# Optimization experiments

Hardware: AMD Instinct MI355X
Metric: run time of the kernel (lower is better)

The kernel has to match this reference:

```python
import jax, jax.numpy as jnp
import numpy as np

N_NODES = 50000
N_EDGES = 800000
D_IN = 128
D_OUT = 128


def setup_inputs() -> dict:
    key = jax.random.key(0)
    k1, k2, k3, k4, k5, k6 = jax.random.split(key, 6)
    embeddings = jax.random.normal(k1, (N_NODES, D_IN), dtype=jnp.float32)
    # kaiming-normal-style scale for the weight
    weight = jax.random.normal(k2, (D_IN, D_OUT), dtype=jnp.float32) * np.sqrt(2.0 / D_IN)
    bias = jax.random.normal(k3, (D_OUT,), dtype=jnp.float32) * 0.01
    edge_val = jax.random.uniform(k4, (N_EDGES,), dtype=jnp.float32)
    edge_row = jax.random.randint(k5, (N_EDGES,), 0, N_NODES, dtype=jnp.int32)
    edge_col = jax.random.randint(k6, (N_EDGES,), 0, N_NODES, dtype=jnp.int32)
    return {
        "embeddings": embeddings,
        "weight": weight,
        "bias": bias,
        "edge_val": edge_val,
        "edge_row": edge_row,
        "edge_col": edge_col,
    }


def reference(embeddings, weight, bias, edge_val, edge_row, edge_col):
    # support = X @ W  -> [N, D_OUT]
    support = jnp.matmul(embeddings, weight)
    # spmm(adj, support): for each edge (r, c, v): out[r] += v * support[c]
    msgs = edge_val[:, None] * support[edge_col]          # [E, D_OUT]
    out = jax.ops.segment_sum(msgs, edge_row, num_segments=embeddings.shape[0])
    return out + bias
```

## Files before the change

kernel.cpp:

```cpp
#include <hip/hip_runtime.h>

#define N_NODES 50000
#define N_EDGES 800000
#define D 128
#define NB 782
#define CHUNK 4096

#define S_OFF      0u
#define GCNT_OFF   12800000u
#define START_OFF  12803200u
#define GCUR_OFF   12806400u
#define OFFS_OFF   12809600u
#define RECS_OFF   13009664u
#define CSR_OFF    19409664u
#define WS_NEEDED  (CSR_OFF + (size_t)N_EDGES * 4u)

__device__ __forceinline__ unsigned bf16_rne(float f) {
    unsigned u = __float_as_uint(f);
    return (u + 0x7fffu + ((u >> 16) & 1u)) >> 16;
}

__global__ __launch_bounds__(512) void gc_gemm(const float* __restrict__ X,
                                               const float* __restrict__ W,
                                               unsigned* __restrict__ Sb) {
    __shared__ float4 LW[4096];
    const int t = threadIdx.x;
    const float4* W4 = (const float4*)W;
    #pragma unroll
    for (int i = 0; i < 8; ++i) LW[t + i * 512] = W4[t + i * 512];
    __syncthreads();

    const int rg = t >> 5;
    const int cg = t & 31;
    const int row0 = blockIdx.x * 64 + rg * 4;
    if (row0 >= N_NODES) return;

    const float4* x0 = (const float4*)(X + (size_t)(row0 + 0) * D);
    const float4* x1 = (const float4*)(X + (size_t)(row0 + 1) * D);
    const float4* x2 = (const float4*)(X + (size_t)(row0 + 2) * D);
    const float4* x3 = (const float4*)(X + (size_t)(row0 + 3) * D);

    float4 a0 = {0.f,0.f,0.f,0.f}, a1 = a0, a2 = a0, a3 = a0;

    #pragma unroll 4
    for (int k4 = 0; k4 < 32; ++k4) {
        float4 xv0 = x0[k4], xv1 = x1[k4], xv2 = x2[k4], xv3 = x3[k4];
        const float* xs0 = (const float*)&xv0;
        const float* xs1 = (const float*)&xv1;
        const float* xs2 = (const float*)&xv2;
        const float* xs3 = (const float*)&xv3;
        #pragma unroll
        for (int kk = 0; kk < 4; ++kk) {
            float4 wv = LW[(k4 * 4 + kk) * 32 + cg];
            float s0 = xs0[kk], s1 = xs1[kk], s2 = xs2[kk], s3 = xs3[kk];
            a0.x += s0 * wv.x; a0.y += s0 * wv.y; a0.z += s0 * wv.z; a0.w += s0 * wv.w;
            a1.x += s1 * wv.x; a1.y += s1 * wv.y; a1.z += s1 * wv.z; a1.w += s1 * wv.w;
            a2.x += s2 * wv.x; a2.y += s2 * wv.y; a2.z += s2 * wv.z; a2.w += s2 * wv.w;
            a3.x += s3 * wv.x; a3.y += s3 * wv.y; a3.z += s3 * wv.z; a3.w += s3 * wv.w;
        }
    }
    uint2* S2 = (uint2*)Sb;
    #define PACK2(f0, f1) (bf16_rne(f0) | (bf16_rne(f1) << 16))
    S2[(size_t)(row0 + 0) * 32 + cg] = make_uint2(PACK2(a0.x, a0.y), PACK2(a0.z, a0.w));
    S2[(size_t)(row0 + 1) * 32 + cg] = make_uint2(PACK2(a1.x, a1.y), PACK2(a1.z, a1.w));
    S2[(size_t)(row0 + 2) * 32 + cg] = make_uint2(PACK2(a2.x, a2.y), PACK2(a2.z, a2.w));
    S2[(size_t)(row0 + 3) * 32 + cg] = make_uint2(PACK2(a3.x, a3.y), PACK2(a3.z, a3.w));
    #undef PACK2
}

__global__ __launch_bounds__(256) void gc_bhist(const int* __restrict__ er,
                                                int* __restrict__ gcnt) {
    __shared__ int h[NB];
    const int t = threadIdx.x;
    for (int b = t; b < NB; b += 256) h[b] = 0;
    __syncthreads();
    for (int e = blockIdx.x * 256 + t; e < N_EDGES; e += gridDim.x * 256)
        atomicAdd(&h[er[e] >> 6], 1);
    __syncthreads();
    for (int b = t; b < NB; b += 256)
        if (h[b]) atomicAdd(&gcnt[b], h[b]);
}

__global__ __launch_bounds__(256) void gc_bscan(const int* __restrict__ gcnt,
                                                int* __restrict__ start,
                                                int* __restrict__ gcursor) {
    __shared__ int sm[256];
    const int t = threadIdx.x;
    int c[4];
    int sum = 0;
    #pragma unroll
    for (int j = 0; j < 4; ++j) {
        int b = t * 4 + j;
        c[j] = (b < NB) ? gcnt[b] : 0;
        sum += c[j];
    }
    sm[t] = sum;
    __syncthreads();
    #pragma unroll
    for (int off = 1; off < 256; off <<= 1) {
        int v = (t >= off) ? sm[t - off] : 0;
        __syncthreads();
        sm[t] += v;
        __syncthreads();
    }
    int excl = sm[t] - sum;
    #pragma unroll
    for (int j = 0; j < 4; ++j) {
        int b = t * 4 + j;
        if (b < NB) { start[b] = excl; gcursor[b] = excl; }
        excl += c[j];
    }
    if (t == 0) start[NB] = N_EDGES;
}

__global__ __launch_bounds__(512) void gc_binscatter(const int* __restrict__ er,
                                                     const int* __restrict__ ec,
                                                     const float* __restrict__ ev,
                                                     int* __restrict__ gcursor,
                                                     uint2* __restrict__ recs) {
    __shared__ uint2 srec[CHUNK];
    __shared__ int cnt[NB];
    __shared__ int base[NB];
    __shared__ int woff[NB];
    __shared__ int gbase[NB];
    __shared__ int sbuf[512];

    const int t = threadIdx.x;
    const int e0 = blockIdx.x * CHUNK;
    const int n = min(CHUNK, N_EDGES - e0);

    for (int b = t; b < NB; b += 512) cnt[b] = 0;
    __syncthreads();

    for (int i = t; i < n; i += 512) atomicAdd(&cnt[er[e0 + i] >> 6], 1);
    __syncthreads();

    int b0 = t * 2, b1 = t * 2 + 1;
    int c0 = (b0 < NB) ? cnt[b0] : 0;
    int c1 = (b1 < NB) ? cnt[b1] : 0;
    int s = c0 + c1;
    sbuf[t] = s;
    __syncthreads();
    #pragma unroll
    for (int off = 1; off < 512; off <<= 1) {
        int v = (t >= off) ? sbuf[t - off] : 0;
        __syncthreads();
        sbuf[t] += v;
        __syncthreads();
    }
    int excl = sbuf[t] - s;
    if (b0 < NB) { base[b0] = excl; woff[b0] = excl; }
    if (b1 < NB) { base[b1] = excl + c0; woff[b1] = excl + c0; }
    __syncthreads();

    for (int i = t; i < n; i += 512) {
        int r = er[e0 + i];
        int c = ec[e0 + i];
        float v = ev[e0 + i];
        int b = r >> 6;
        int pos = atomicAdd(&woff[b], 1);
        srec[pos] = make_uint2(((unsigned)c << 16) | bf16_rne(v), (unsigned)r);
    }
    __syncthreads();

    for (int b = t; b < NB; b += 512)
        if (cnt[b]) gbase[b] = atomicAdd(&gcursor[b], cnt[b]);
    __syncthreads();

    for (int i = t; i < n; i += 512) {
        uint2 rec = srec[i];
        int b = (int)(rec.y >> 6);
        recs[gbase[b] + (i - base[b])] = rec;
    }
}

__global__ __launch_bounds__(256) void gc_bsort(const uint2* __restrict__ recs,
                                                const int* __restrict__ start,
                                                int* __restrict__ offsets,
                                                unsigned* __restrict__ csr) {
    __shared__ int h[64];
    __shared__ int cur[64];
    const int b = blockIdx.x;
    const int t = threadIdx.x;
    const int s = start[b];
    const int e = start[b + 1];

    if (t < 64) h[t] = 0;
    __syncthreads();

    for (int i = s + t; i < e; i += 256)
        atomicAdd(&h[recs[i].y & 63], 1);
    __syncthreads();

    if (t < 64) {
        int hv = h[t];
        int v = hv;
        #pragma unroll
        for (int off = 1; off < 64; off <<= 1) {
            int u = __shfl_up(v, off);
            if (t >= off) v += u;
        }
        int ex = s + v - hv;
        cur[t] = ex;
        int grow = b * 64 + t;
        if (grow < N_NODES) offsets[grow] = ex;
        if (grow == N_NODES - 1 || (b == NB - 1 && t == 63))
            offsets[N_NODES] = N_EDGES;
    }
    __syncthreads();

    for (int i = s + t; i < e; i += 256) {
        uint2 r = recs[i];
        int pos = atomicAdd(&cur[r.y & 63], 1);
        csr[pos] = r.x;
    }
}

__global__ void gc_gather(const unsigned* __restrict__ Sb,
                          const int* __restrict__ offsets,
                          const unsigned* __restrict__ csr,
                          const float* __restrict__ bias,
                          float* __restrict__ out) {
    int wid  = (blockIdx.x * blockDim.x + threadIdx.x) >> 6;
    int lane = threadIdx.x & 63;
    if (wid >= N_NODES) return;

    int start = offsets[wid];
    int end   = offsets[wid + 1];

    float ax0 = 0.f, ay0 = 0.f, ax1 = 0.f, ay1 = 0.f;
    int e = start;
    for (; e + 3 < end; e += 4) {
        unsigned cv0 = csr[e];
        unsigned cv1 = csr[e + 1];
        unsigned cv2 = csr[e + 2];
        unsigned cv3 = csr[e + 3];
        unsigned s0 = Sb[(size_t)(cv0 >> 16) * 64 + lane];
        unsigned s1 = Sb[(size_t)(cv1 >> 16) * 64 + lane];
        unsigned s2 = Sb[(size_t)(cv2 >> 16) * 64 + lane];
        unsigned s3 = Sb[(size_t)(cv3 >> 16) * 64 + lane];
        float v0 = __uint_as_float(cv0 << 16);
        float v1 = __uint_as_float(cv1 << 16);
        float v2 = __uint_as_float(cv2 << 16);
        float v3 = __uint_as_float(cv3 << 16);
        ax0 += v0 * __uint_as_float(s0 << 16);
        ay0 += v0 * __uint_as_float(s0 & 0xffff0000u);
        ax1 += v1 * __uint_as_float(s1 << 16);
        ay1 += v1 * __uint_as_float(s1 & 0xffff0000u);
        ax0 += v2 * __uint_as_float(s2 << 16);
        ay0 += v2 * __uint_as_float(s2 & 0xffff0000u);
        ax1 += v3 * __uint_as_float(s3 << 16);
        ay1 += v3 * __uint_as_float(s3 & 0xffff0000u);
    }
    for (; e < end; ++e) {
        unsigned cv = csr[e];
        unsigned s = Sb[(size_t)(cv >> 16) * 64 + lane];
        float v = __uint_as_float(cv << 16);
        ax0 += v * __uint_as_float(s << 16);
        ay0 += v * __uint_as_float(s & 0xffff0000u);
    }

    float2 b = *(const float2*)(bias + lane * 2);
    float2 r = make_float2(ax0 + ax1 + b.x, ay0 + ay1 + b.y);
    *(float2*)(out + (size_t)wid * D + lane * 2) = r;
}

extern "C" void kernel_launch(void* const* d_in, const int* in_sizes, int n_in,
                              void* d_out, int out_size, void* d_ws, size_t ws_size,
                              hipStream_t stream) {
    const float* X    = (const float*)d_in[0];
    const float* W    = (const float*)d_in[1];
    const float* bias = (const float*)d_in[2];
    const float* ev   = (const float*)d_in[3];
    const int*   er   = (const int*)  d_in[4];
    const int*   ec   = (const int*)  d_in[5];
    float* out = (float*)d_out;

    char* ws = (char*)d_ws;
    unsigned* Sb      = (unsigned*)(ws + S_OFF);
    int*      gcnt    = (int*)(ws + GCNT_OFF);
    int*      start   = (int*)(ws + START_OFF);
    int*      gcursor = (int*)(ws + GCUR_OFF);
    int*      offsets = (int*)(ws + OFFS_OFF);
    uint2*    recs    = (uint2*)(ws + RECS_OFF);
    unsigned* csr     = (unsigned*)(ws + CSR_OFF);

    gc_gemm<<<(N_NODES + 63) / 64, 512, 0, stream>>>(X, W, Sb);

    hipMemsetAsync(gcnt, 0, NB * sizeof(int), stream);

    gc_bhist<<<256, 256, 0, stream>>>(er, gcnt);
    gc_bscan<<<1, 256, 0, stream>>>(gcnt, start, gcursor);
    gc_binscatter<<<(N_EDGES + CHUNK - 1) / CHUNK, 512, 0, stream>>>(er, ec, ev, gcursor, recs);
    gc_bsort<<<NB, 256, 0, stream>>>(recs, start, offsets, csr);

    int gblocks = (N_NODES * 64 + 255) / 256;
    gc_gather<<<gblocks, 256, 0, stream>>>(Sb, offsets, csr, bias, out);
}
```

Baseline: 191.9 us.

## Replace FP32 SIMT GEMM with bf16 MFMA matrix-core GEMM

Rewrites the X@W projection to use 16x16x32 bf16 MFMA instructions. W is converted to bf16 and stored transposed and padded in shared memory, and each wave computes a 16x128 tile. This is meant to remove the scalar FMA cost of the dense GEMM stage. In exchange, X and W are now rounded to bf16 before multiplying, which lowers precision; the output stores are scattered 2-byte writes, and the last block may read rows past N_NODES.

```diff
diff --git a/kernel.cpp b/kernel.cpp
--- a/kernel.cpp
+++ b/kernel.cpp
@@ -15,57 +15,77 @@
 #define CSR_OFF    19409664u
 #define WS_NEEDED  (CSR_OFF + (size_t)N_EDGES * 4u)
 
+typedef __attribute__((ext_vector_type(8))) short bf16x8;
+typedef __attribute__((ext_vector_type(4))) float f32x4;
+
 __device__ __forceinline__ unsigned bf16_rne(float f) {
     unsigned u = __float_as_uint(f);
     return (u + 0x7fffu + ((u >> 16) & 1u)) >> 16;
 }
 
-__global__ __launch_bounds__(512) void gc_gemm(const float* __restrict__ X,
-                                               const float* __restrict__ W,
-                                               unsigned* __restrict__ Sb) {
-    __shared__ float4 LW[4096];
-    const int t = threadIdx.x;
-    const float4* W4 = (const float4*)W;
-    #pragma unroll
-    for (int i = 0; i < 8; ++i) LW[t + i * 512] = W4[t + i * 512];
-    __syncthreads();
-
-    const int rg = t >> 5;
-    const int cg = t & 31;
-    const int row0 = blockIdx.x * 64 + rg * 4;
+__global__ __launch_bounds__(256) void gc_gemm_mfma(const float* __restrict__ X,
+                                                    const float* __restrict__ W,
+                                                    ushort* __restrict__ Sb16) {
+    __shared__ unsigned lwtU[128 * 68];
+    const ushort* lwt = (const ushort*)lwtU;
+
+    const int t = threadIdx.x;
+    {
+        const int n  = t >> 1;
+        const int kb = (t & 1) * 64;
+        #pragma unroll
+        for (int i = 0; i < 32; ++i) {
+            int k = kb + 2 * i;
+            unsigned lo = bf16_rne(W[(size_t)k * 128 + n]);
+            unsigned hi = bf16_rne(W[(size_t)(k + 1) * 128 + n]);
+            lwtU[n * 68 + (k >> 1)] = lo | (hi << 16);
+        }
+    }
+    __syncthreads();
+
+    const int wv   = t >> 6;
+    const int lane = t & 63;
+    const int g    = lane >> 4;
+    const int lm   = lane & 15;
+    const int row0 = blockIdx.x * 64 + wv * 16;
     if (row0 >= N_NODES) return;
 
-    const float4* x0 = (const float4*)(X + (size_t)(row0 + 0) * D);
-    const float4* x1 = (const float4*)(X + (size_t)(row0 + 1) * D);
-    const float4* x2 = (const float4*)(X + (size_t)(row0 + 2) * D);
-    const float4* x3 = (const float4*)(X + (size_t)(row0 + 3) * D);
-
-    float4 a0 = {0.f,0.f,0.f,0.f}, a1 = a0, a2 = a0, a3 = a0;
-
-    #pragma unroll 4
-    for (int k4 = 0; k4 < 32; ++k4) {
-        float4 xv0 = x0[k4], xv1 = x1[k4], xv2 = x2[k4], xv3 = x3[k4];
-        const float* xs0 = (const float*)&xv0;
-        const float* xs1 = (const float*)&xv1;
-        const float* xs2 = (const float*)&xv2;
-        const float* xs3 = (const float*)&xv3;
+    const int row = row0 + lm;
+    const float4* xr = (const float4*)(X + (size_t)row * 128);
+
+    f32x4 acc[8];
+    #pragma unroll
+    for (int i = 0; i < 8; ++i) acc[i] = (f32x4){0.f, 0.f, 0.f, 0.f};
+
+    #pragma unroll
+    for (int ks = 0; ks < 4; ++ks) {
+        float4 x0 = xr[ks * 8 + g];
+        float4 x1 = xr[ks * 8 + 4 + g];
+        bf16x8 a;
+        a[0] = (short)bf16_rne(x0.x); a[1] = (short)bf16_rne(x0.y);
+        a[2] = (short)bf16_rne(x0.z); a[3] = (short)bf16_rne(x0.w);
+        a[4] = (short)bf16_rne(x1.x); a[5] = (short)bf16_rne(x1.y);
+        a[6] = (short)bf16_rne(x1.z); a[7] = (short)bf16_rne(x1.w);
+        const int kk0 = ks * 32 + 4 * g;
         #pragma unroll
-        for (int kk = 0; kk < 4; ++kk) {
-            float4 wv = LW[(k4 * 4 + kk) * 32 + cg];
-            float s0 = xs0[kk], s1 = xs1[kk], s2 = xs2[kk], s3 = xs3[kk];
-            a0.x += s0 * wv.x; a0.y += s0 * wv.y; a0.z += s0 * wv.z; a0.w += s0 * wv.w;
-            a1.x += s1 * wv.x; a1.y += s1 * wv.y; a1.z += s1 * wv.z; a1.w += s1 * wv.w;
-            a2.x += s2 * wv.x; a2.y += s2 * wv.y; a2.z += s2 * wv.z; a2.w += s2 * wv.w;
-            a3.x += s3 * wv.x; a3.y += s3 * wv.y; a3.z += s3 * wv.z; a3.w += s3 * wv.w;
+        for (int nt = 0; nt < 8; ++nt) {
+            const int n = nt * 16 + lm;
+            short4 b0 = *(const short4*)&lwt[n * 136 + kk0];
+            short4 b1 = *(const short4*)&lwt[n * 136 + kk0 + 16];
+            bf16x8 b;
+            b[0] = b0.x; b[1] = b0.y; b[2] = b0.z; b[3] = b0.w;
+            b[4] = b1.x; b[5] = b1.y; b[6] = b1.z; b[7] = b1.w;
+            acc[nt] = __builtin_amdgcn_mfma_f32_16x16x32_bf16(a, b, acc[nt], 0, 0, 0);
         }
     }
-    uint2* S2 = (uint2*)Sb;
-    #define PACK2(f0, f1) (bf16_rne(f0) | (bf16_rne(f1) << 16))
-    S2[(size_t)(row0 + 0) * 32 + cg] = make_uint2(PACK2(a0.x, a0.y), PACK2(a0.z, a0.w));
-    S2[(size_t)(row0 + 1) * 32 + cg] = make_uint2(PACK2(a1.x, a1.y), PACK2(a1.z, a1.w));
-    S2[(size_t)(row0 + 2) * 32 + cg] = make_uint2(PACK2(a2.x, a2.y), PACK2(a2.z, a2.w));
-    S2[(size_t)(row0 + 3) * 32 + cg] = make_uint2(PACK2(a3.x, a3.y), PACK2(a3.z, a3.w));
-    #undef PACK2
+
+    #pragma unroll
+    for (int r = 0; r < 4; ++r) {
+        ushort* orow = Sb16 + (size_t)(row0 + 4 * g + r) * 128;
+        #pragma unroll
+        for (int nt = 0; nt < 8; ++nt)
+            orow[nt * 16 + lm] = (ushort)bf16_rne(acc[nt][r]);
+    }
 }
 
 __global__ __launch_bounds__(256) void gc_bhist(const int* __restrict__ er,
@@ -277,6 +297,7 @@
     float* out = (float*)d_out;
 
     char* ws = (char*)d_ws;
+    ushort*   Sb16    = (ushort*)(ws + S_OFF);
     unsigned* Sb      = (unsigned*)(ws + S_OFF);
     int*      gcnt    = (int*)(ws + GCNT_OFF);
     int*      start   = (int*)(ws + START_OFF);
@@ -285,7 +306,7 @@
     uint2*    recs    = (uint2*)(ws + RECS_OFF);
     unsigned* csr     = (unsigned*)(ws + CSR_OFF);
 
-    gc_gemm<<<(N_NODES + 63) / 64, 512, 0, stream>>>(X, W, Sb);
+    gc_gemm_mfma<<<(N_NODES + 63) / 64, 256, 0, stream>>>(X, W, Sb16);
 
     hipMemsetAsync(gcnt, 0, NB * sizeof(int), stream);
 
```

After: 169.0 us. -11.9%, faster.
